# Kernel tuning notes

Measured on AMD Instinct MI355X. Metric: run time of the kernel, lower is better.

Reference implementation:

```python
import jax, jax.numpy as jnp
import numpy as np


def setup_inputs() -> dict:
    key = jax.random.key(0)
    k_u, k_a, k_b, k_c, k_d = jax.random.split(key, 5)
    n_dim, m_dim, p_dim = 1024, 1024, 1024
    batch, T = 8, 2048
    u = jax.random.normal(k_u, (batch, T, m_dim), dtype=jnp.float32)
    A = jax.random.normal(k_a, (n_dim, n_dim), dtype=jnp.float32) / np.sqrt(n_dim).astype(np.float32)
    B = jax.random.normal(k_b, (n_dim, m_dim), dtype=jnp.float32)
    C = jax.random.normal(k_c, (p_dim, n_dim), dtype=jnp.float32)
    D = jax.random.normal(k_d, (p_dim, m_dim), dtype=jnp.float32)
    return {"u": u, "A": A, "B": B, "C": C, "D": D}


def reference(u, A, B, C, D):
    # NOTE: torch.einsum('bn,nn->bn', x, A.T) with repeated label 'n' on the
    # second operand takes the DIAGONAL of A. So the recurrence is
    #   x_k = x_{k-1} * diag(A) + u_k @ B^T
    #   y_k = x_k @ C^T + u_k @ D^T
    a = jnp.diagonal(A)  # (n,)
    # Precompute time-invariant input projection in one big GEMM: (b, T, n)
    Bu = jnp.einsum('btm,nm->btn', u, B)
    batch = u.shape[0]
    x0 = jnp.zeros((batch, a.shape[0]), dtype=u.dtype)

    def step(x, bu_k):
        x = x * a + bu_k
        return x, x

    # scan over time: Bu transposed to (T, b, n)
    _, X = jax.lax.scan(step, x0, jnp.swapaxes(Bu, 0, 1))
    X = jnp.swapaxes(X, 0, 1)  # (b, T, n)
    y = jnp.einsum('btn,pn->btp', X, C) + jnp.einsum('btm,pm->btp', u, D)
    return y
```

## Files before the change

### kernel.cpp

```cpp
#include <hip/hip_runtime.h>
#include <hip/hip_bf16.h>
#include <stdint.h>


typedef __attribute__((ext_vector_type(8))) short short8;
typedef __attribute__((ext_vector_type(4))) float floatx4;

#define BM 128
#define BN 128
#define BK 32

__device__ __forceinline__ uint16_t f2bf(float f) {
    union { float f; uint32_t u; } v; v.f = f;
    uint32_t u = v.u;
    return (uint16_t)((u + 0x7FFFu + ((u >> 16) & 1u)) >> 16);
}

__device__ __forceinline__ uint32_t pk_bf16(float x, float y) {
    union { __hip_bfloat162 h; uint32_t u; } v;
    v.h = __float22bfloat162_rn(make_float2(x, y));
    return v.u;
}

__device__ __forceinline__ float bf2f(uint16_t b) {
    union { uint32_t u; float f; } v; v.u = ((uint32_t)b) << 16;
    return v.f;
}

__global__ void cvt_f32_bf16(const float* __restrict__ src, uint16_t* __restrict__ dst, int n4) {
    int i = blockIdx.x * blockDim.x + threadIdx.x;
    if (i < n4) {
        float4 v = ((const float4*)src)[i];
        uint2 o;
        o.x = pk_bf16(v.x, v.y);
        o.y = pk_bf16(v.z, v.w);
        ((uint2*)dst)[i] = o;
    }
}

#define CHUNK 128
#define LOOKBACK 64
__global__ void scan_kernel(const uint16_t* __restrict__ Bu, const float* __restrict__ Amat,
                            uint16_t* __restrict__ Xbf, int T, int Nn) {
    int n = blockIdx.z * blockDim.x + threadIdx.x;
    int b = blockIdx.y;
    int chunk = blockIdx.x;
    float a = Amat[(size_t)n * Nn + n];
    const uint16_t* bu = Bu + ((size_t)b * T) * Nn + n;
    uint16_t* xp = Xbf + ((size_t)b * T) * Nn + n;
    int t0 = chunk * CHUNK;
    int ts = t0 - LOOKBACK; if (ts < 0) ts = 0;
    float x = 0.f;
    for (int t = ts; t < t0; ++t) x = x * a + bf2f(bu[(size_t)t * Nn]);
    for (int t = t0; t < t0 + CHUNK; ++t) {
        x = x * a + bf2f(bu[(size_t)t * Nn]);
        xp[(size_t)t * Nn] = f2bf(x);
    }
}

template <bool W_FP32, bool OUT_BF16>
__global__ void gemm_bt(const uint16_t* __restrict__ A0, const void* __restrict__ W0v,
                        const uint16_t* __restrict__ A1, const void* __restrict__ W1v,
                        void* __restrict__ Cout, int M, int N, int K, int nseg,
                        int bx_off) {
    __shared__ alignas(16) uint16_t As[BM * BK];
    __shared__ alignas(16) uint16_t Bs[BN * BK];

    const int tid  = threadIdx.x;
    const int wave = tid >> 6;
    const int lane = tid & 63;
    const int quad = lane >> 4;
    const int l16  = lane & 15;
    const int m0 = (blockIdx.x + bx_off) * BM;
    const int n0 = blockIdx.y * BN;
    const int wr = (wave >> 1) * 64;
    const int wc = (wave & 1) * 64;

    floatx4 acc[4][4];
#pragma unroll
    for (int i = 0; i < 4; ++i)
#pragma unroll
        for (int j = 0; j < 4; ++j) acc[i][j] = (floatx4)(0.f);

    for (int seg = 0; seg < nseg; ++seg) {
        const uint16_t* A = seg ? A1 : A0;
        const void* Wv = seg ? W1v : W0v;
        const float* Wf = (const float*)Wv;
        const uint16_t* Wb = (const uint16_t*)Wv;

        float4 wreg[4];
        if (W_FP32) {
#pragma unroll
            for (int r = 0; r < 4; ++r) {
                int row = r * 32 + (tid >> 3);
                int col = (tid & 7) * 4;
                wreg[r] = *(const float4*)(Wf + (size_t)(n0 + row) * K + col);
            }
        }

        for (int k0 = 0; k0 < K; k0 += BK) {
            __syncthreads();
#pragma unroll
            for (int r = 0; r < 2; ++r) {
                int L = r * 256 + tid;
                int row = L >> 2;
                int col = (L & 3) * 8;
                const uint16_t* gp = A + (size_t)(m0 + row) * K + k0 + col;
                uint16_t* lb = &As[(size_t)(r * 256 + wave * 64) * 8];
                __builtin_amdgcn_global_load_lds(
                    (const __attribute__((address_space(1))) void*)gp,
                    (__attribute__((address_space(3))) void*)lb, 16, 0, 0);
            }
            if (W_FP32) {
#pragma unroll
                for (int r = 0; r < 4; ++r) {
                    int row = r * 32 + (tid >> 3);
                    int col = (tid & 7) * 4;
                    uint2 o;
                    o.x = pk_bf16(wreg[r].x, wreg[r].y);
                    o.y = pk_bf16(wreg[r].z, wreg[r].w);
                    *(uint2*)&Bs[row * BK + col] = o;
                }
                if (k0 + BK < K) {
#pragma unroll
                    for (int r = 0; r < 4; ++r) {
                        int row = r * 32 + (tid >> 3);
                        int col = (tid & 7) * 4;
                        wreg[r] = *(const float4*)(Wf + (size_t)(n0 + row) * K + k0 + BK + col);
                    }
                }
            } else {
#pragma unroll
                for (int r = 0; r < 2; ++r) {
                    int L = r * 256 + tid;
                    int row = L >> 2;
                    int col = (L & 3) * 8;
                    const uint16_t* gp = Wb + (size_t)(n0 + row) * K + k0 + col;
                    uint16_t* lb = &Bs[(size_t)(r * 256 + wave * 64) * 8];
                    __builtin_amdgcn_global_load_lds(
                        (const __attribute__((address_space(1))) void*)gp,
                        (__attribute__((address_space(3))) void*)lb, 16, 0, 0);
                }
            }
            __syncthreads();

            short8 af[4], bf[4];
#pragma unroll
            for (int i = 0; i < 4; ++i)
                af[i] = *(const short8*)&As[(wr + i * 16 + l16) * BK + quad * 8];
#pragma unroll
            for (int j = 0; j < 4; ++j)
                bf[j] = *(const short8*)&Bs[(wc + j * 16 + l16) * BK + quad * 8];
#pragma unroll
            for (int i = 0; i < 4; ++i)
#pragma unroll
                for (int j = 0; j < 4; ++j)
                    acc[i][j] = __builtin_amdgcn_mfma_f32_16x16x32_bf16(
                        af[i], bf[j], acc[i][j], 0, 0, 0);
        }
    }

#pragma unroll
    for (int i = 0; i < 4; ++i)
#pragma unroll
        for (int j = 0; j < 4; ++j)
#pragma unroll
            for (int r = 0; r < 4; ++r) {
                int row = m0 + wr + i * 16 + quad * 4 + r;
                int col = n0 + wc + j * 16 + l16;
                if (OUT_BF16)
                    ((uint16_t*)Cout)[(size_t)row * N + col] = f2bf(acc[i][j][r]);
                else
                    ((float*)Cout)[(size_t)row * N + col] = acc[i][j][r];
            }
}

extern "C" void kernel_launch(void* const* d_in, const int* in_sizes, int n_in,
                              void* d_out, int out_size, void* d_ws, size_t ws_size,
                              hipStream_t stream) {
    const float* u = (const float*)d_in[0];
    const float* A = (const float*)d_in[1];
    const float* B = (const float*)d_in[2];
    const float* C = (const float*)d_in[3];
    const float* D = (const float*)d_in[4];
    float* y = (float*)d_out;

    const int batch = 8, T = 2048, Kd = 1024, Nd = 1024;
    const int M = batch * T;
    const size_t MB = 1024 * 1024;

    uint16_t* u_bf = (uint16_t*)d_ws;
    uint16_t* X_bf = u_bf + (size_t)M * Kd;
    uint16_t* B_bf = X_bf;
    uint16_t* Bu_bf = (uint16_t*)d_out;

    const int n4u = (M * Kd) / 4;
    const int n4w = (Nd * Kd) / 4;

    cvt_f32_bf16<<<n4u / 256, 256, 0, stream>>>(u, u_bf, n4u);
    cvt_f32_bf16<<<n4w / 256, 256, 0, stream>>>(B, B_bf, n4w);

    if (ws_size >= 68 * MB) {
        uint16_t* C_bf = X_bf + (size_t)M * Nd;
        uint16_t* D_bf = C_bf + (size_t)Nd * Kd;
        cvt_f32_bf16<<<n4w / 256, 256, 0, stream>>>(C, C_bf, n4w);
        cvt_f32_bf16<<<n4w / 256, 256, 0, stream>>>(D, D_bf, n4w);

        gemm_bt<false, true><<<dim3(M / BM, Nd / BN), 256, 0, stream>>>(
            u_bf, B_bf, nullptr, nullptr, Bu_bf, M, Nd, Kd, 1, 0);
        scan_kernel<<<dim3(T / CHUNK, batch, Nd / 256), 256, 0, stream>>>(
            Bu_bf, A, X_bf, T, Nd);
        gemm_bt<false, false><<<dim3(M / BM, Nd / BN), 256, 0, stream>>>(
            X_bf, C_bf, u_bf, D_bf, y, M, Nd, Kd, 2, 0);
    } else {
        uint16_t* C_bf = (uint16_t*)((char*)d_out + 60 * MB);
        uint16_t* D_bf = (uint16_t*)((char*)d_out + 62 * MB);
        cvt_f32_bf16<<<n4w / 256, 256, 0, stream>>>(C, C_bf, n4w);
        cvt_f32_bf16<<<n4w / 256, 256, 0, stream>>>(D, D_bf, n4w);

        gemm_bt<false, true><<<dim3(M / BM, Nd / BN), 256, 0, stream>>>(
            u_bf, B_bf, nullptr, nullptr, Bu_bf, M, Nd, Kd, 1, 0);

        scan_kernel<<<dim3(T / CHUNK, batch, Nd / 256), 256, 0, stream>>>(
            Bu_bf, A, X_bf, T, Nd);

        gemm_bt<false, false><<<dim3(120, Nd / BN), 256, 0, stream>>>(
            X_bf, C_bf, u_bf, D_bf, y, M, Nd, Kd, 2, 0);
        gemm_bt<true, false><<<dim3(8, Nd / BN), 256, 0, stream>>>(
            X_bf, C, u_bf, D, y, M, Nd, Kd, 2, 120);
    }
}
```

Before: 282.8 us.

## Fuse conversions, vectorize scan, stage C/D in output with grid-wide arrival barrier

Merges the four fp32-to-bf16 conversion launches into one kernel and makes the scan handle two channels per thread with 32-bit loads and stores. The final GEMM always keeps bf16 C and D inside the output buffer, which removes the separate fp32-weight GEMM path. To avoid overwriting those weights before every block has read them, blocks whose output tiles overlap the staging region wait on a global atomic counter until all blocks have finished their main loop. The blocks are also relinearized into a 1D grid with the N dimension fastest, for better weight reuse. The spin barrier assumes all blocks can make progress together, which risks deadlock or stalls if they are not all resident at once.

```diff
diff --git a/kernel.cpp b/kernel.cpp
--- a/kernel.cpp
+++ b/kernel.cpp
@@ -27,42 +27,60 @@
     return v.f;
 }
 
-__global__ void cvt_f32_bf16(const float* __restrict__ src, uint16_t* __restrict__ dst, int n4) {
+__global__ void cvt_all(const float* __restrict__ u, const float* __restrict__ B,
+                        const float* __restrict__ C, const float* __restrict__ D,
+                        uint16_t* __restrict__ u_bf, uint16_t* __restrict__ B_bf,
+                        uint16_t* __restrict__ C_bf, uint16_t* __restrict__ D_bf,
+                        unsigned* __restrict__ counter, int n4u, int n4w) {
     int i = blockIdx.x * blockDim.x + threadIdx.x;
-    if (i < n4) {
-        float4 v = ((const float4*)src)[i];
-        uint2 o;
-        o.x = pk_bf16(v.x, v.y);
-        o.y = pk_bf16(v.z, v.w);
-        ((uint2*)dst)[i] = o;
-    }
+    if (i == 0) *counter = 0u;
+    const float* src; uint16_t* dst; int idx;
+    if (i < n4u)                { src = u; dst = u_bf; idx = i; }
+    else if (i < n4u + n4w)     { src = B; dst = B_bf; idx = i - n4u; }
+    else if (i < n4u + 2 * n4w) { src = C; dst = C_bf; idx = i - n4u - n4w; }
+    else if (i < n4u + 3 * n4w) { src = D; dst = D_bf; idx = i - n4u - 2 * n4w; }
+    else return;
+    float4 v = ((const float4*)src)[idx];
+    uint2 o;
+    o.x = pk_bf16(v.x, v.y);
+    o.y = pk_bf16(v.z, v.w);
+    ((uint2*)dst)[idx] = o;
 }
 
 #define CHUNK 128
 #define LOOKBACK 64
 __global__ void scan_kernel(const uint16_t* __restrict__ Bu, const float* __restrict__ Amat,
                             uint16_t* __restrict__ Xbf, int T, int Nn) {
-    int n = blockIdx.z * blockDim.x + threadIdx.x;
+    int n2 = blockIdx.z * blockDim.x + threadIdx.x;
+    int n = n2 * 2;
     int b = blockIdx.y;
     int chunk = blockIdx.x;
-    float a = Amat[(size_t)n * Nn + n];
-    const uint16_t* bu = Bu + ((size_t)b * T) * Nn + n;
-    uint16_t* xp = Xbf + ((size_t)b * T) * Nn + n;
+    float a0 = Amat[(size_t)n * Nn + n];
+    float a1 = Amat[(size_t)(n + 1) * Nn + n + 1];
+    const uint32_t* bu = (const uint32_t*)(Bu + ((size_t)b * T) * Nn) + n2;
+    uint32_t* xp = (uint32_t*)(Xbf + ((size_t)b * T) * Nn) + n2;
+    const int halfN = Nn >> 1;
     int t0 = chunk * CHUNK;
     int ts = t0 - LOOKBACK; if (ts < 0) ts = 0;
-    float x = 0.f;
-    for (int t = ts; t < t0; ++t) x = x * a + bf2f(bu[(size_t)t * Nn]);
+    float x0 = 0.f, x1 = 0.f;
+    for (int t = ts; t < t0; ++t) {
+        uint32_t w = bu[(size_t)t * halfN];
+        x0 = x0 * a0 + bf2f((uint16_t)w);
+        x1 = x1 * a1 + bf2f((uint16_t)(w >> 16));
+    }
     for (int t = t0; t < t0 + CHUNK; ++t) {
-        x = x * a + bf2f(bu[(size_t)t * Nn]);
-        xp[(size_t)t * Nn] = f2bf(x);
-    }
-}
-
-template <bool W_FP32, bool OUT_BF16>
-__global__ void gemm_bt(const uint16_t* __restrict__ A0, const void* __restrict__ W0v,
-                        const uint16_t* __restrict__ A1, const void* __restrict__ W1v,
+        uint32_t w = bu[(size_t)t * halfN];
+        x0 = x0 * a0 + bf2f((uint16_t)w);
+        x1 = x1 * a1 + bf2f((uint16_t)(w >> 16));
+        xp[(size_t)t * halfN] = pk_bf16(x0, x1);
+    }
+}
+
+template <bool OUT_BF16, bool ARRIVE>
+__global__ void gemm_bt(const uint16_t* __restrict__ A0, const uint16_t* __restrict__ W0,
+                        const uint16_t* __restrict__ A1, const uint16_t* __restrict__ W1,
                         void* __restrict__ Cout, int M, int N, int K, int nseg,
-                        int bx_off) {
+                        unsigned* counter) {
     __shared__ alignas(16) uint16_t As[BM * BK];
     __shared__ alignas(16) uint16_t Bs[BN * BK];
 
@@ -71,8 +89,11 @@
     const int lane = tid & 63;
     const int quad = lane >> 4;
     const int l16  = lane & 15;
-    const int m0 = (blockIdx.x + bx_off) * BM;
-    const int n0 = blockIdx.y * BN;
+    const int lid  = blockIdx.x;
+    const int by   = lid & 7;
+    const int bx   = lid >> 3;
+    const int m0 = bx * BM;
+    const int n0 = by * BN;
     const int wr = (wave >> 1) * 64;
     const int wc = (wave & 1) * 64;
 
@@ -84,20 +105,7 @@
 
     for (int seg = 0; seg < nseg; ++seg) {
         const uint16_t* A = seg ? A1 : A0;
-        const void* Wv = seg ? W1v : W0v;
-        const float* Wf = (const float*)Wv;
-        const uint16_t* Wb = (const uint16_t*)Wv;
-
-        float4 wreg[4];
-        if (W_FP32) {
-#pragma unroll
-            for (int r = 0; r < 4; ++r) {
-                int row = r * 32 + (tid >> 3);
-                int col = (tid & 7) * 4;
-                wreg[r] = *(const float4*)(Wf + (size_t)(n0 + row) * K + col);
-            }
-        }
-
+        const uint16_t* W = seg ? W1 : W0;
         for (int k0 = 0; k0 < K; k0 += BK) {
             __syncthreads();
 #pragma unroll
@@ -111,36 +119,16 @@
                     (const __attribute__((address_space(1))) void*)gp,
                     (__attribute__((address_space(3))) void*)lb, 16, 0, 0);
             }
-            if (W_FP32) {
-#pragma unroll
-                for (int r = 0; r < 4; ++r) {
-                    int row = r * 32 + (tid >> 3);
-                    int col = (tid & 7) * 4;
-                    uint2 o;
-                    o.x = pk_bf16(wreg[r].x, wreg[r].y);
-                    o.y = pk_bf16(wreg[r].z, wreg[r].w);
-                    *(uint2*)&Bs[row * BK + col] = o;
-                }
-                if (k0 + BK < K) {
-#pragma unroll
-                    for (int r = 0; r < 4; ++r) {
-                        int row = r * 32 + (tid >> 3);
-                        int col = (tid & 7) * 4;
-                        wreg[r] = *(const float4*)(Wf + (size_t)(n0 + row) * K + k0 + BK + col);
-                    }
-                }
-            } else {
-#pragma unroll
-                for (int r = 0; r < 2; ++r) {
-                    int L = r * 256 + tid;
-                    int row = L >> 2;
-                    int col = (L & 3) * 8;
-                    const uint16_t* gp = Wb + (size_t)(n0 + row) * K + k0 + col;
-                    uint16_t* lb = &Bs[(size_t)(r * 256 + wave * 64) * 8];
-                    __builtin_amdgcn_global_load_lds(
-                        (const __attribute__((address_space(1))) void*)gp,
-                        (__attribute__((address_space(3))) void*)lb, 16, 0, 0);
-                }
+#pragma unroll
+            for (int r = 0; r < 2; ++r) {
+                int L = r * 256 + tid;
+                int row = L >> 2;
+                int col = (L & 3) * 8;
+                const uint16_t* gp = W + (size_t)(n0 + row) * K + k0 + col;
+                uint16_t* lb = &Bs[(size_t)(r * 256 + wave * 64) * 8];
+                __builtin_amdgcn_global_load_lds(
+                    (const __attribute__((address_space(1))) void*)gp,
+                    (__attribute__((address_space(3))) void*)lb, 16, 0, 0);
             }
             __syncthreads();
 
@@ -158,6 +146,24 @@
                     acc[i][j] = __builtin_amdgcn_mfma_f32_16x16x32_bf16(
                         af[i], bf[j], acc[i][j], 0, 0, 0);
         }
+    }
+
+    if (ARRIVE) {
+        __syncthreads();
+        const int nbx = (int)(gridDim.x >> 3);
+        bool spinner = (bx >= nbx - 8) || (bx == nbx - 9 && by == 7);
+        if (tid == 0) {
+            __threadfence();
+            __hip_atomic_fetch_add(counter, 1u, __ATOMIC_RELEASE,
+                                   __HIP_MEMORY_SCOPE_AGENT);
+            if (spinner) {
+                while (__hip_atomic_load(counter, __ATOMIC_ACQUIRE,
+                                         __HIP_MEMORY_SCOPE_AGENT) < gridDim.x) {
+                    __builtin_amdgcn_s_sleep(32);
+                }
+            }
+        }
+        if (spinner) __syncthreads();
     }
 
 #pragma unroll
@@ -193,40 +199,22 @@
     uint16_t* X_bf = u_bf + (size_t)M * Kd;
     uint16_t* B_bf = X_bf;
     uint16_t* Bu_bf = (uint16_t*)d_out;
+    uint16_t* C_bf = (uint16_t*)((char*)d_out + 60 * MB);
+    uint16_t* D_bf = (uint16_t*)((char*)d_out + 62 * MB);
+    unsigned* counter = (unsigned*)((char*)d_out + 60 * MB - 4);
 
     const int n4u = (M * Kd) / 4;
     const int n4w = (Nd * Kd) / 4;
 
-    cvt_f32_bf16<<<n4u / 256, 256, 0, stream>>>(u, u_bf, n4u);
-    cvt_f32_bf16<<<n4w / 256, 256, 0, stream>>>(B, B_bf, n4w);
-
-    if (ws_size >= 68 * MB) {
-        uint16_t* C_bf = X_bf + (size_t)M * Nd;
-        uint16_t* D_bf = C_bf + (size_t)Nd * Kd;
-        cvt_f32_bf16<<<n4w / 256, 256, 0, stream>>>(C, C_bf, n4w);
-        cvt_f32_bf16<<<n4w / 256, 256, 0, stream>>>(D, D_bf, n4w);
-
-        gemm_bt<false, true><<<dim3(M / BM, Nd / BN), 256, 0, stream>>>(
-            u_bf, B_bf, nullptr, nullptr, Bu_bf, M, Nd, Kd, 1, 0);
-        scan_kernel<<<dim3(T / CHUNK, batch, Nd / 256), 256, 0, stream>>>(
-            Bu_bf, A, X_bf, T, Nd);
-        gemm_bt<false, false><<<dim3(M / BM, Nd / BN), 256, 0, stream>>>(
-            X_bf, C_bf, u_bf, D_bf, y, M, Nd, Kd, 2, 0);
-    } else {
-        uint16_t* C_bf = (uint16_t*)((char*)d_out + 60 * MB);
-        uint16_t* D_bf = (uint16_t*)((char*)d_out + 62 * MB);
-        cvt_f32_bf16<<<n4w / 256, 256, 0, stream>>>(C, C_bf, n4w);
-        cvt_f32_bf16<<<n4w / 256, 256, 0, stream>>>(D, D_bf, n4w);
-
-        gemm_bt<false, true><<<dim3(M / BM, Nd / BN), 256, 0, stream>>>(
-            u_bf, B_bf, nullptr, nullptr, Bu_bf, M, Nd, Kd, 1, 0);
-
-        scan_kernel<<<dim3(T / CHUNK, batch, Nd / 256), 256, 0, stream>>>(
-            Bu_bf, A, X_bf, T, Nd);
-
-        gemm_bt<false, false><<<dim3(120, Nd / BN), 256, 0, stream>>>(
-            X_bf, C_bf, u_bf, D_bf, y, M, Nd, Kd, 2, 0);
-        gemm_bt<true, false><<<dim3(8, Nd / BN), 256, 0, stream>>>(
-            X_bf, C, u_bf, D, y, M, Nd, Kd, 2, 120);
-    }
-}
+    cvt_all<<<(n4u + 3 * n4w) / 256, 256, 0, stream>>>(
+        u, B, C, D, u_bf, B_bf, C_bf, D_bf, counter, n4u, n4w);
+
+    gemm_bt<true, false><<<(M / BM) * (Nd / BN), 256, 0, stream>>>(
+        u_bf, B_bf, nullptr, nullptr, Bu_bf, M, Nd, Kd, 1, nullptr);
+
+    scan_kernel<<<dim3(T / CHUNK, batch, Nd / 512), 256, 0, stream>>>(
+        Bu_bf, A, X_bf, T, Nd);
+
+    gemm_bt<false, true><<<(M / BM) * (Nd / BN), 256, 0, stream>>>(
+        X_bf, C_bf, u_bf, D_bf, y, M, Nd, Kd, 2, counter);
+}
```

Result: slower. 372.5 us (+31.7%).
